# Kernel optimization log

Hardware: AMD Instinct MI355X
Metric: run time of the kernel (lower is better)

The kernel has to match this reference:

```python
import jax, jax.numpy as jnp
import numpy as np

NUM_EXPERT = 8
IN_FEAT = 1024
OUT_FEAT = 1024
N_TOKENS = 8192


def setup_inputs() -> dict:
    key = jax.random.key(0)
    k_inp, k_gate, k_w = jax.random.split(key, 3)
    inp = jax.random.normal(k_inp, (N_TOKENS, IN_FEAT), dtype=jnp.float32)
    gate = jax.random.randint(k_gate, (N_TOKENS,), 0, NUM_EXPERT, dtype=jnp.int32)
    # FMoELinear weight: [num_expert, out_feat, in_feat], kaiming-uniform-like init
    bound = 1.0 / np.sqrt(IN_FEAT)
    weight = jax.random.uniform(
        k_w, (NUM_EXPERT, OUT_FEAT, IN_FEAT), dtype=jnp.float32,
        minval=-bound, maxval=bound)
    return {"inp": inp, "gate": gate, "weight": weight}


def reference(inp, gate, weight):
    # out[i] = weight[gate[i]] @ inp[i]  (top-1 MoE dispatch + grouped GEMM + combine)
    # Loop over the small fixed expert set via scan; each step does a masked
    # dense GEMM so only tokens routed to expert e contribute.
    n, _ = inp.shape
    num_expert, out_feat, _ = weight.shape

    def body(acc, ew):
        e, w_e = ew  # w_e: [out_feat, in_feat]
        mask = (gate == e).astype(inp.dtype)[:, None]  # [n, 1]
        acc = acc + (inp * mask) @ w_e.T               # [n, out_feat]
        return acc, None

    init = jnp.zeros((n, out_feat), dtype=inp.dtype)
    out, _ = jax.lax.scan(body, init, (jnp.arange(num_expert), weight))
    return out
```

## Files before the change

kernel.cpp:

```cpp
#include <hip/hip_runtime.h>
#include <hip/hip_bf16.h>

#define N_TOKENS 8192
#define IN_FEAT 1024
#define OUT_FEAT 1024
#define NUM_EXPERT 8

#define BM 128
#define BN 128
#define BK 32

typedef __bf16 bf16x8 __attribute__((ext_vector_type(8)));
typedef float f32x4 __attribute__((ext_vector_type(4)));

__device__ __forceinline__ unsigned int rne16(float x) {
    union { float f; unsigned int u; } c;
    c.f = x;
    unsigned int u = c.u;
    u += 0x7fffu + ((u >> 16) & 1u);
    return u >> 16;
}
__device__ __forceinline__ unsigned int pk2(float x, float y) {
    return rne16(x) | (rne16(y) << 16);
}

__device__ __forceinline__ void load_lds16(const void* g, void* l) {
    __builtin_amdgcn_global_load_lds(
        (const __attribute__((address_space(1))) unsigned int*)g,
        (__attribute__((address_space(3))) unsigned int*)l,
        16, 0, 0);
}


__global__ __launch_bounds__(256) void moe_hist(const int* __restrict__ gate,
                                                int* __restrict__ cnt) {
    __shared__ int lc[NUM_EXPERT];
    const int t = threadIdx.x;
    if (t < NUM_EXPERT) lc[t] = 0;
    __syncthreads();
    int g = gate[blockIdx.x * 256 + t];
    atomicAdd(&lc[g], 1);
    __syncthreads();
    if (t < NUM_EXPERT) atomicAdd(&cnt[t], lc[t]);
}

__global__ void moe_scan(const int* __restrict__ cnt, int* __restrict__ seg,
                         int* __restrict__ cur) {
    int s = 0;
    #pragma unroll
    for (int e = 0; e < NUM_EXPERT; ++e) { seg[e] = s; cur[e] = s; s += cnt[e]; }
    seg[NUM_EXPERT] = s;
}

__global__ __launch_bounds__(256) void moe_scatter(const int* __restrict__ gate,
                                                   int* __restrict__ cur,
                                                   int* __restrict__ perm) {
    const int t = threadIdx.x;
    const int lane = t & 63;
    const unsigned long long lt = (lane == 0) ? 0ull : (~0ull >> (64 - lane));
    const int i = blockIdx.x * 256 + t;
    int g = gate[i];
    #pragma unroll
    for (int e = 0; e < NUM_EXPERT; ++e) {
        unsigned long long m = __ballot(g == e);
        if (g == e) {
            int rank = __popcll(m & lt);
            int leader = (int)__ffsll((unsigned long long)m) - 1;
            int p0 = 0;
            if (rank == 0) p0 = atomicAdd(&cur[e], __popcll(m));
            p0 = __shfl(p0, leader);
            perm[p0 + rank] = i;
        }
    }
}

__global__ __launch_bounds__(256) void moe_prep(const float* __restrict__ inp,
                                                const float* __restrict__ weight,
                                                const int* __restrict__ perm,
                                                unsigned int* __restrict__ A2,
                                                unsigned int* __restrict__ W2) {
    const int bid = blockIdx.x;
    const int t = threadIdx.x;
    const int wave = t >> 6, lane = t & 63;
    const float* src;
    unsigned int* dst;
    if (bid < 2048) {
        int row = bid * 4 + wave;
        src = inp + perm[row] * IN_FEAT;
        dst = A2 + row * (IN_FEAT / 2);
    } else {
        int row = (bid - 2048) * 4 + wave;
        src = weight + row * IN_FEAT;
        dst = W2 + row * (IN_FEAT / 2);
    }
    #pragma unroll
    for (int j = 0; j < 4; ++j) {
        float4 v = *(const float4*)(src + j * 256 + lane * 4);
        uint2 o;
        o.x = pk2(v.x, v.y);
        o.y = pk2(v.z, v.w);
        *(uint2*)(dst + j * 128 + lane * 2) = o;
    }
}

__global__ __launch_bounds__(256, 4) void moe_gemm(
    const unsigned short* __restrict__ A2,
    const unsigned short* __restrict__ W2,
    const int* __restrict__ perm,
    const int* __restrict__ seg,
    float* __restrict__ out) {

    const int bid = blockIdx.x;
    const int e = bid & 7;
    const int ntile = (bid >> 3) & 7;
    const int mtile = bid >> 6;

    const int base = seg[e];
    const int cnt = seg[e + 1] - base;
    if (mtile * BM >= cnt) return;
    const int tbase = base + mtile * BM;
    int rows = cnt - mtile * BM; if (rows > BM) rows = BM;

    __shared__ __align__(16) unsigned short lA[2][BM * BK];
    __shared__ __align__(16) unsigned short lB[2][BN * BK];

    const int t = threadIdx.x;

    const int crow = t >> 2;
    const int p = (t & 3) ^ (crow & 3);
    int ar0 = tbase + crow;       if (ar0 > N_TOKENS - 1) ar0 = N_TOKENS - 1;
    int ar1 = tbase + 64 + crow;  if (ar1 > N_TOKENS - 1) ar1 = N_TOKENS - 1;
    const unsigned short* gA0 = A2 + ar0 * IN_FEAT + p * 8;
    const unsigned short* gA1 = A2 + ar1 * IN_FEAT + p * 8;
    const unsigned short* gB0 = W2 + e * (OUT_FEAT * IN_FEAT)
                                + (ntile * BN + crow) * IN_FEAT + p * 8;
    const unsigned short* gB1 = gB0 + 64 * IN_FEAT;
    const int dofs = t * 8;
    const int dofs2 = (t + 256) * 8;

    const int wave = t >> 6;
    const int lane = t & 63;
    const int wm = (wave & 1) << 6;
    const int wn = (wave >> 1) << 6;
    const int l15 = lane & 15;
    const int quad = lane >> 4;
    const int qx = quad ^ (l15 & 3);
    const int fofsA = (wm + l15) * BK + qx * 8;
    const int fofsB = (wn + l15) * BK + qx * 8;

    f32x4 acc[4][4];
    #pragma unroll
    for (int i = 0; i < 4; ++i)
        #pragma unroll
        for (int j = 0; j < 4; ++j)
            acc[i][j] = (f32x4)0.0f;

    load_lds16(gA0, &lA[0][dofs]);
    load_lds16(gA1, &lA[0][dofs2]);
    load_lds16(gB0, &lB[0][dofs]);
    load_lds16(gB1, &lB[0][dofs2]);

    #pragma unroll 1
    for (int kk = 0; kk < 16; ++kk) {
        const int k0 = kk * 64;

        __syncthreads();
        load_lds16(gA0 + k0 + 32, &lA[1][dofs]);
        load_lds16(gA1 + k0 + 32, &lA[1][dofs2]);
        load_lds16(gB0 + k0 + 32, &lB[1][dofs]);
        load_lds16(gB1 + k0 + 32, &lB[1][dofs2]);

        {
            bf16x8 af[4], bq[4];
            #pragma unroll
            for (int i = 0; i < 4; ++i)
                af[i] = *(const bf16x8*)&lA[0][fofsA + i * 16 * BK];
            #pragma unroll
            for (int j = 0; j < 4; ++j)
                bq[j] = *(const bf16x8*)&lB[0][fofsB + j * 16 * BK];
            #pragma unroll
            for (int i = 0; i < 4; ++i)
                #pragma unroll
                for (int j = 0; j < 4; ++j)
                    acc[i][j] = __builtin_amdgcn_mfma_f32_16x16x32_bf16(
                        af[i], bq[j], acc[i][j], 0, 0, 0);
        }

        __syncthreads();
        if (kk < 15) {
            load_lds16(gA0 + k0 + 64, &lA[0][dofs]);
            load_lds16(gA1 + k0 + 64, &lA[0][dofs2]);
            load_lds16(gB0 + k0 + 64, &lB[0][dofs]);
            load_lds16(gB1 + k0 + 64, &lB[0][dofs2]);
        }

        {
            bf16x8 af[4], bq[4];
            #pragma unroll
            for (int i = 0; i < 4; ++i)
                af[i] = *(const bf16x8*)&lA[1][fofsA + i * 16 * BK];
            #pragma unroll
            for (int j = 0; j < 4; ++j)
                bq[j] = *(const bf16x8*)&lB[1][fofsB + j * 16 * BK];
            #pragma unroll
            for (int i = 0; i < 4; ++i)
                #pragma unroll
                for (int j = 0; j < 4; ++j)
                    acc[i][j] = __builtin_amdgcn_mfma_f32_16x16x32_bf16(
                        af[i], bq[j], acc[i][j], 0, 0, 0);
        }
    }

    #pragma unroll
    for (int mi = 0; mi < 4; ++mi) {
        #pragma unroll
        for (int r = 0; r < 4; ++r) {
            int row = wm + mi * 16 + quad * 4 + r;
            if (row < rows) {
                int token = perm[tbase + row];
                float* op = out + token * OUT_FEAT + ntile * BN + wn;
                #pragma unroll
                for (int ni = 0; ni < 4; ++ni)
                    op[ni * 16 + l15] = acc[mi][ni][r];
            }
        }
    }
}

#define FLDSW 20
__global__ __launch_bounds__(256, 4) void moe_gemm_fb(
    const float* __restrict__ inp,
    const float* __restrict__ weight,
    const int* __restrict__ perm,
    const int* __restrict__ seg,
    float* __restrict__ out) {

    const int bid = blockIdx.x;
    const int mtile = bid >> 7;
    const int e = (bid >> 4) & 7;
    const int ntile = bid & 15;

    const int base = seg[e];
    const int cnt = seg[e + 1] - base;
    if (mtile * 128 >= cnt) return;

    __shared__ unsigned int lA[128 * FLDSW];
    __shared__ unsigned int lB[64 * FLDSW];
    __shared__ int rowids[128];

    const int t = threadIdx.x;
    if (t < 128) {
        int r = mtile * 128 + t;
        rowids[t] = (r < cnt) ? perm[base + r] : -1;
    }
    __syncthreads();

    const int srow = t >> 1;
    const int scol = (t & 1) << 4;
    const int tokA = rowids[srow];
    const bool aval = (tokA >= 0);
    const float* aptr = inp + (aval ? tokA : 0) * IN_FEAT + scol;
    const int sdstA = srow * FLDSW + (scol >> 1);
    const int browB = t >> 2;
    const int bcol = (t & 3) << 3;
    const float* bptr = weight + e * (OUT_FEAT * IN_FEAT)
                        + (ntile * 64 + browB) * IN_FEAT + bcol;
    const int sdstB = browB * FLDSW + (bcol >> 1);

    const int wave = t >> 6;
    const int lane = t & 63;
    const int wm = (wave & 1) << 6;
    const int wn = (wave >> 1) << 5;
    const int l15 = lane & 15;
    const int quad = lane >> 4;

    f32x4 acc[4][2];
    #pragma unroll
    for (int i = 0; i < 4; ++i)
        #pragma unroll
        for (int j = 0; j < 2; ++j)
            acc[i][j] = (f32x4)0.0f;

    float4 ra[4], rb[2];
    {
        const float4* ap = (const float4*)aptr;
        const float4* bp = (const float4*)bptr;
        #pragma unroll
        for (int i = 0; i < 4; ++i) ra[i] = ap[i];
        #pragma unroll
        for (int i = 0; i < 2; ++i) rb[i] = bp[i];
    }

    for (int k0 = 0; k0 < IN_FEAT; k0 += 32) {
        unsigned int ua[8], ub[4];
        #pragma unroll
        for (int i = 0; i < 4; ++i) {
            ua[2 * i]     = pk2(ra[i].x, ra[i].y);
            ua[2 * i + 1] = pk2(ra[i].z, ra[i].w);
        }
        #pragma unroll
        for (int i = 0; i < 2; ++i) {
            ub[2 * i]     = pk2(rb[i].x, rb[i].y);
            ub[2 * i + 1] = pk2(rb[i].z, rb[i].w);
        }
        if (!aval) {
            #pragma unroll
            for (int i = 0; i < 8; ++i) ua[i] = 0u;
        }

        __syncthreads();
        *(uint4*)&lA[sdstA]     = make_uint4(ua[0], ua[1], ua[2], ua[3]);
        *(uint4*)&lA[sdstA + 4] = make_uint4(ua[4], ua[5], ua[6], ua[7]);
        *(uint4*)&lB[sdstB]     = make_uint4(ub[0], ub[1], ub[2], ub[3]);
        __syncthreads();

        if (k0 + 32 < IN_FEAT) {
            const float4* ap = (const float4*)(aptr + k0 + 32);
            const float4* bp = (const float4*)(bptr + k0 + 32);
            #pragma unroll
            for (int i = 0; i < 4; ++i) ra[i] = ap[i];
            #pragma unroll
            for (int i = 0; i < 2; ++i) rb[i] = bp[i];
        }

        bf16x8 af[4], bq[2];
        #pragma unroll
        for (int i = 0; i < 4; ++i)
            af[i] = *(const bf16x8*)&lA[(wm + i * 16 + l15) * FLDSW + (quad << 2)];
        #pragma unroll
        for (int j = 0; j < 2; ++j)
            bq[j] = *(const bf16x8*)&lB[(wn + j * 16 + l15) * FLDSW + (quad << 2)];

        #pragma unroll
        for (int i = 0; i < 4; ++i)
            #pragma unroll
            for (int j = 0; j < 2; ++j)
                acc[i][j] = __builtin_amdgcn_mfma_f32_16x16x32_bf16(
                    af[i], bq[j], acc[i][j], 0, 0, 0);
    }

    #pragma unroll
    for (int mi = 0; mi < 4; ++mi) {
        #pragma unroll
        for (int r = 0; r < 4; ++r) {
            int row = wm + mi * 16 + quad * 4 + r;
            int token = rowids[row];
            if (token >= 0) {
                float* op = out + token * OUT_FEAT + ntile * 64 + wn;
                #pragma unroll
                for (int ni = 0; ni < 2; ++ni)
                    op[ni * 16 + l15] = acc[mi][ni][r];
            }
        }
    }
}

extern "C" void kernel_launch(void* const* d_in, const int* in_sizes, int n_in,
                              void* d_out, int out_size, void* d_ws, size_t ws_size,
                              hipStream_t stream) {
    const float* inp = (const float*)d_in[0];
    const int* gate = (const int*)d_in[1];
    const float* weight = (const float*)d_in[2];
    float* out = (float*)d_out;

    int* perm = (int*)d_ws;
    int* seg = perm + N_TOKENS;
    int* cnt = seg + 16;
    int* cur = cnt + 8;

    hipMemsetAsync(cnt, 0, 16 * sizeof(int), stream);
    moe_hist<<<N_TOKENS / 256, 256, 0, stream>>>(gate, cnt);
    moe_scan<<<1, 1, 0, stream>>>(cnt, seg, cur);
    moe_scatter<<<N_TOKENS / 256, 256, 0, stream>>>(gate, cur, perm);

    const size_t need = 65536 + 2ull * N_TOKENS * IN_FEAT * 2;
    if (ws_size >= need) {
        unsigned int* A2 = (unsigned int*)((char*)d_ws + 65536);
        unsigned int* W2 = A2 + (N_TOKENS * IN_FEAT / 2);
        moe_prep<<<4096, 256, 0, stream>>>(inp, weight, perm, A2, W2);
        moe_gemm<<<4096, 256, 0, stream>>>((const unsigned short*)A2,
                                           (const unsigned short*)W2,
                                           perm, seg, out);
    } else {
        moe_gemm_fb<<<8192, 256, 0, stream>>>(inp, weight, perm, seg, out);
    }
}
```

Measured before the change: 152.4 us.

## Fuse routing sort into prep kernel with single-block sort and gemm-side gather

Replaces the memset plus histogram, scan and scatter kernels with a single-block ballot-based counting sort. On the fast path that sort runs as block 0 of the prep kernel, so it overlaps with the bf16 conversion. The prep kernel now converts input rows in their original order, and the GEMM gathers A rows through perm when it loads. This removes three kernel launches and a memset, plus the serial dependency between sorting and conversion. In exchange the sort runs on one block, which is slow, and the GEMM now does indirect row addressing through perm.

```diff
diff --git a/kernel.cpp b/kernel.cpp
--- a/kernel.cpp
+++ b/kernel.cpp
@@ -31,65 +31,107 @@
         16, 0, 0);
 }
 
-
-__global__ __launch_bounds__(256) void moe_hist(const int* __restrict__ gate,
-                                                int* __restrict__ cnt) {
-    __shared__ int lc[NUM_EXPERT];
+__device__ __forceinline__ void sort_block256(const int* __restrict__ gate,
+                                              int* __restrict__ perm,
+                                              int* __restrict__ seg) {
+    __shared__ int whist[4][NUM_EXPERT];
+    __shared__ int wbase[4][NUM_EXPERT];
     const int t = threadIdx.x;
-    if (t < NUM_EXPERT) lc[t] = 0;
+    const int wave = t >> 6, lane = t & 63;
+    const unsigned long long lt = (lane == 0) ? 0ull : (~0ull >> (64 - lane));
+
+    int4 v[8];
+    #pragma unroll
+    for (int j = 0; j < 8; ++j)
+        v[j] = ((const int4*)gate)[j * 256 + t];
+
+    int cnt[NUM_EXPERT];
+    #pragma unroll
+    for (int e = 0; e < NUM_EXPERT; ++e) cnt[e] = 0;
+    #pragma unroll
+    for (int j = 0; j < 8; ++j) {
+        #pragma unroll
+        for (int q = 0; q < 4; ++q) {
+            const int g = (q == 0) ? v[j].x : (q == 1) ? v[j].y
+                        : (q == 2) ? v[j].z : v[j].w;
+            #pragma unroll
+            for (int e = 0; e < NUM_EXPERT; ++e) {
+                unsigned long long m = __ballot(g == e);
+                cnt[e] += (int)__popcll(m);
+            }
+        }
+    }
+    if (lane == 0) {
+        #pragma unroll
+        for (int e = 0; e < NUM_EXPERT; ++e) whist[wave][e] = cnt[e];
+    }
     __syncthreads();
-    int g = gate[blockIdx.x * 256 + t];
-    atomicAdd(&lc[g], 1);
+
+    if (t == 0) {
+        int s = 0;
+        #pragma unroll
+        for (int e = 0; e < NUM_EXPERT; ++e) {
+            seg[e] = s;
+            int b = s;
+            #pragma unroll
+            for (int w = 0; w < 4; ++w) { wbase[w][e] = b; b += whist[w][e]; }
+            s = b;
+        }
+        seg[NUM_EXPERT] = s;
+    }
     __syncthreads();
-    if (t < NUM_EXPERT) atomicAdd(&cnt[t], lc[t]);
-}
-
-__global__ void moe_scan(const int* __restrict__ cnt, int* __restrict__ seg,
-                         int* __restrict__ cur) {
-    int s = 0;
-    #pragma unroll
-    for (int e = 0; e < NUM_EXPERT; ++e) { seg[e] = s; cur[e] = s; s += cnt[e]; }
-    seg[NUM_EXPERT] = s;
-}
-
-__global__ __launch_bounds__(256) void moe_scatter(const int* __restrict__ gate,
-                                                   int* __restrict__ cur,
-                                                   int* __restrict__ perm) {
-    const int t = threadIdx.x;
-    const int lane = t & 63;
-    const unsigned long long lt = (lane == 0) ? 0ull : (~0ull >> (64 - lane));
-    const int i = blockIdx.x * 256 + t;
-    int g = gate[i];
-    #pragma unroll
-    for (int e = 0; e < NUM_EXPERT; ++e) {
-        unsigned long long m = __ballot(g == e);
-        if (g == e) {
-            int rank = __popcll(m & lt);
-            int leader = (int)__ffsll((unsigned long long)m) - 1;
-            int p0 = 0;
-            if (rank == 0) p0 = atomicAdd(&cur[e], __popcll(m));
-            p0 = __shfl(p0, leader);
-            perm[p0 + rank] = i;
-        }
-    }
-}
-
-__global__ __launch_bounds__(256) void moe_prep(const float* __restrict__ inp,
-                                                const float* __restrict__ weight,
-                                                const int* __restrict__ perm,
-                                                unsigned int* __restrict__ A2,
-                                                unsigned int* __restrict__ W2) {
+
+    int off[NUM_EXPERT];
+    #pragma unroll
+    for (int e = 0; e < NUM_EXPERT; ++e) off[e] = wbase[wave][e];
+    #pragma unroll
+    for (int j = 0; j < 8; ++j) {
+        #pragma unroll
+        for (int q = 0; q < 4; ++q) {
+            const int g = (q == 0) ? v[j].x : (q == 1) ? v[j].y
+                        : (q == 2) ? v[j].z : v[j].w;
+            const int tok = j * 1024 + t * 4 + q;
+            #pragma unroll
+            for (int e = 0; e < NUM_EXPERT; ++e) {
+                unsigned long long m = __ballot(g == e);
+                if (g == e) perm[off[e] + (int)__popcll(m & lt)] = tok;
+                off[e] += (int)__popcll(m);
+            }
+        }
+    }
+}
+
+__global__ __launch_bounds__(256) void moe_sort(const int* __restrict__ gate,
+                                                int* __restrict__ perm,
+                                                int* __restrict__ seg) {
+    sort_block256(gate, perm, seg);
+}
+
+__global__ __launch_bounds__(256) void moe_prep_sort(
+    const float* __restrict__ inp,
+    const float* __restrict__ weight,
+    const int* __restrict__ gate,
+    int* __restrict__ perm,
+    int* __restrict__ seg,
+    unsigned int* __restrict__ A2,
+    unsigned int* __restrict__ W2) {
+
     const int bid = blockIdx.x;
+    if (bid == 0) {
+        sort_block256(gate, perm, seg);
+        return;
+    }
+    const int cid = bid - 1;
     const int t = threadIdx.x;
     const int wave = t >> 6, lane = t & 63;
     const float* src;
     unsigned int* dst;
-    if (bid < 2048) {
-        int row = bid * 4 + wave;
-        src = inp + perm[row] * IN_FEAT;
+    if (cid < 2048) {
+        int row = cid * 4 + wave;
+        src = inp + row * IN_FEAT;
         dst = A2 + row * (IN_FEAT / 2);
     } else {
-        int row = (bid - 2048) * 4 + wave;
+        int row = (cid - 2048) * 4 + wave;
         src = weight + row * IN_FEAT;
         dst = W2 + row * (IN_FEAT / 2);
     }
@@ -130,8 +172,10 @@
     const int p = (t & 3) ^ (crow & 3);
     int ar0 = tbase + crow;       if (ar0 > N_TOKENS - 1) ar0 = N_TOKENS - 1;
     int ar1 = tbase + 64 + crow;  if (ar1 > N_TOKENS - 1) ar1 = N_TOKENS - 1;
-    const unsigned short* gA0 = A2 + ar0 * IN_FEAT + p * 8;
-    const unsigned short* gA1 = A2 + ar1 * IN_FEAT + p * 8;
+    const int pr0 = perm[ar0];
+    const int pr1 = perm[ar1];
+    const unsigned short* gA0 = A2 + (size_t)pr0 * IN_FEAT + p * 8;
+    const unsigned short* gA1 = A2 + (size_t)pr1 * IN_FEAT + p * 8;
     const unsigned short* gB0 = W2 + e * (OUT_FEAT * IN_FEAT)
                                 + (ntile * BN + crow) * IN_FEAT + p * 8;
     const unsigned short* gB1 = gB0 + 64 * IN_FEAT;
@@ -365,23 +409,18 @@
 
     int* perm = (int*)d_ws;
     int* seg = perm + N_TOKENS;
-    int* cnt = seg + 16;
-    int* cur = cnt + 8;
-
-    hipMemsetAsync(cnt, 0, 16 * sizeof(int), stream);
-    moe_hist<<<N_TOKENS / 256, 256, 0, stream>>>(gate, cnt);
-    moe_scan<<<1, 1, 0, stream>>>(cnt, seg, cur);
-    moe_scatter<<<N_TOKENS / 256, 256, 0, stream>>>(gate, cur, perm);
 
     const size_t need = 65536 + 2ull * N_TOKENS * IN_FEAT * 2;
     if (ws_size >= need) {
         unsigned int* A2 = (unsigned int*)((char*)d_ws + 65536);
         unsigned int* W2 = A2 + (N_TOKENS * IN_FEAT / 2);
-        moe_prep<<<4096, 256, 0, stream>>>(inp, weight, perm, A2, W2);
+        moe_prep_sort<<<4097, 256, 0, stream>>>(inp, weight, gate, perm, seg,
+                                                A2, W2);
         moe_gemm<<<4096, 256, 0, stream>>>((const unsigned short*)A2,
                                            (const unsigned short*)W2,
                                            perm, seg, out);
     } else {
+        moe_sort<<<1, 256, 0, stream>>>(gate, perm, seg);
         moe_gemm_fb<<<8192, 256, 0, stream>>>(inp, weight, perm, seg, out);
     }
 }
```

New measurement: 142.7 us. -6.4%, faster.
